# Kernel optimization log

Hardware: AMD Instinct MI355X
Metric: run time of the kernel (lower is better)

## Reference

```python
import jax, jax.numpy as jnp
import numpy as np


def setup_inputs() -> dict:
    key = jax.random.key(0)
    ks = jax.random.split(key, 6)
    B, HW, CIN, COUT, K = 256, 64, 3, 128, 32
    inputs = jax.random.normal(ks[0], (B, HW, HW, CIN), jnp.float32)
    conv_w = jax.random.normal(ks[1], (3, 3, CIN, COUT), jnp.float32) * 0.1
    conv_b = jnp.zeros((COUT,), jnp.float32)
    match_w = jax.random.normal(ks[2], (COUT,), jnp.float32) * 0.1
    match_b = jnp.zeros((1,), jnp.float32)
    pat_w = jax.random.normal(ks[3], (32 * 32 * K, 1), jnp.float32) * 0.01
    pat_b = jnp.zeros((1,), jnp.float32)
    base_w = jax.random.normal(ks[4], (32 * 32 * COUT, 3), jnp.float32) * 0.01
    base_b = jnp.zeros((3,), jnp.float32)
    pattern_set_index = jax.random.randint(ks[5], (K,), 0, COUT, jnp.int32)
    return {
        "inputs": inputs, "conv_w": conv_w, "conv_b": conv_b,
        "match_w": match_w, "match_b": match_b,
        "pat_w": pat_w, "pat_b": pat_b,
        "base_w": base_w, "base_b": base_b,
        "pattern_set_index": pattern_set_index,
    }


def reference(inputs, conv_w, conv_b, match_w, match_b,
              pat_w, pat_b, base_w, base_b, pattern_set_index):
    B = inputs.shape[0]
    # feat_extract: conv3x3 stride 2 + relu -> feats0 [B,32,32,128]; GAP -> feats1 [B,128]
    feats0 = jax.nn.relu(
        jax.lax.conv_general_dilated(
            inputs, conv_w, window_strides=(2, 2), padding='SAME',
            dimension_numbers=('NHWC', 'HWIO', 'NHWC')) + conv_b)
    feats1 = feats0.mean(axis=(1, 2))  # [B,128]
    # pat_matcher: boolean per-sample match mask
    matches = (feats1 @ match_w + match_b[0]) > 0.0  # [B] bool
    # pat_pred on channel-subset features (tf.gather axis=3)
    sel = jnp.take(feats0, pattern_set_index, axis=3)  # [B,32,32,32]
    p = jax.nn.sigmoid(sel.reshape(B, -1) @ pat_w + pat_b)[:, 0]  # [B]
    # BinaryToCategorical(pattern_class=0, num_classes=3): [p, (1-p)/2, (1-p)/2]
    o = (1.0 - p) * 0.5
    cat = jnp.stack([p, o, o], axis=-1)  # [B,3]
    # base_pred on full features (used for matched-low and non-matched samples)
    base = jax.nn.softmax(feats0.reshape(B, -1) @ base_w + base_b, axis=-1)  # [B,3]
    # route: matched AND pat score >= 0.5 -> categorized pat pred, else base pred
    use_pat = matches & (p >= 0.5)
    return jnp.where(use_pat[:, None], cat, base)
```

## Files before the change

### kernel.cpp

```cpp
#include <hip/hip_runtime.h>
#include <math.h>

#define TPB 1024

__global__ __launch_bounds__(256)
void prep_weights(const float* __restrict__ base_w,
                  const float* __restrict__ pat_w,
                  const int*   __restrict__ psi,
                  float4* __restrict__ wq)
{
    int idx = blockIdx.x * 256 + threadIdx.x;
    int hw = idx >> 7, c = idx & 127;
    const float* bp = base_w + (size_t)idx * 3;
    float b0 = bp[0], b1 = bp[1], b2 = bp[2];
    float pc = 0.f;
    const float* pr = pat_w + hw * 32;
    #pragma unroll
    for (int k = 0; k < 32; ++k)
        pc += (psi[k] == c) ? pr[k] : 0.f;
    wq[idx] = make_float4(b0, b1, b2, pc);
}

__global__ __launch_bounds__(TPB, 4)
void pattern_branch_kernel(const float* __restrict__ in,
                           const float* __restrict__ conv_w,
                           const float* __restrict__ conv_b,
                           const float* __restrict__ match_w,
                           const float* __restrict__ match_b,
                           const float* __restrict__ pat_b,
                           const float* __restrict__ base_b,
                           const float4* __restrict__ wq,
                           float* __restrict__ out)
{
    constexpr int ROWF4 = 50;
    __shared__ float4 xlds4[65 * ROWF4];
    __shared__ float  red[16][5];

    const int b   = blockIdx.x;
    const int tid = threadIdx.x;

    for (int s = tid; s < 65 * ROWF4; s += TPB) xlds4[s] = make_float4(0.f, 0.f, 0.f, 0.f);
    __syncthreads();
    const float4* inp4 = (const float4*)(in + (size_t)b * 12288);
    for (int s = tid; s < 64 * 48; s += TPB) {
        int r = s / 48;
        int q = s - r * 48;
        xlds4[r * ROWF4 + q] = inp4[s];
    }
    __syncthreads();

    const int lane31 = tid & 31;
    const int cg     = (tid >> 5) & 1;
    const int sg     = tid >> 6;
    const int c0     = lane31 + 32 * cg;
    float w[2][27], bias[2], mw[2];
    #pragma unroll
    for (int jj = 0; jj < 2; ++jj) {
        int c = c0 + 64 * jj;
        bias[jj] = conv_b[c];
        mw[jj]   = match_w[c];
        #pragma unroll
        for (int k = 0; k < 27; ++k) w[jj][k] = conv_w[k * 128 + c];
    }

    float s_match = 0.f, sb0 = 0.f, sb1 = 0.f, sb2 = 0.f, s_pat = 0.f;

    for (int it = 0; it < 16; ++it) {
        int slot = it * 16 + sg;
        int oh = slot >> 3;
        int q  = slot & 7;
        float acc[4][2];
        #pragma unroll
        for (int v = 0; v < 4; ++v) { acc[v][0] = bias[0]; acc[v][1] = bias[1]; }

        #pragma unroll
        for (int kh = 0; kh < 3; ++kh) {
            float xr[28];
            const float4* rp = &xlds4[(2 * oh + kh) * ROWF4 + 6 * q];
            #pragma unroll
            for (int u = 0; u < 7; ++u) {
                float4 v4 = rp[u];
                xr[4*u] = v4.x; xr[4*u+1] = v4.y; xr[4*u+2] = v4.z; xr[4*u+3] = v4.w;
            }
            #pragma unroll
            for (int v = 0; v < 4; ++v)
                #pragma unroll
                for (int t9 = 0; t9 < 9; ++t9) {
                    float xv = xr[6 * v + t9];
                    int k = kh * 9 + t9;
                    acc[v][0] = fmaf(xv, w[0][k], acc[v][0]);
                    acc[v][1] = fmaf(xv, w[1][k], acc[v][1]);
                }
        }
        #pragma unroll
        for (int v = 0; v < 4; ++v) {
            int hw = oh * 32 + 4 * q + v;
            const float4* wqp = wq + hw * 128 + c0;
            #pragma unroll
            for (int jj = 0; jj < 2; ++jj) {
                float fv = fmaxf(acc[v][jj], 0.f);
                float4 wv = wqp[64 * jj];
                s_match = fmaf(mw[jj], fv, s_match);
                sb0   = fmaf(fv, wv.x, sb0);
                sb1   = fmaf(fv, wv.y, sb1);
                sb2   = fmaf(fv, wv.z, sb2);
                s_pat = fmaf(fv, wv.w, s_pat);
            }
        }
    }

    float vals[5] = { s_match, sb0, sb1, sb2, s_pat };
    #pragma unroll
    for (int off = 32; off > 0; off >>= 1)
        #pragma unroll
        for (int v = 0; v < 5; ++v)
            vals[v] += __shfl_down(vals[v], off, 64);
    int wv = tid >> 6, lane = tid & 63;
    if (lane == 0) {
        #pragma unroll
        for (int v = 0; v < 5; ++v) red[wv][v] = vals[v];
    }
    __syncthreads();
    if (tid == 0) {
        float t[5] = {0.f, 0.f, 0.f, 0.f, 0.f};
        for (int wj = 0; wj < 16; ++wj)
            #pragma unroll
            for (int v = 0; v < 5; ++v) t[v] += red[wj][v];
        float score = t[0] * (1.f / 1024.f) + match_b[0];
        float p = 1.f / (1.f + expf(-(t[4] + pat_b[0])));
        float l0 = t[1] + base_b[0], l1 = t[2] + base_b[1], l2 = t[3] + base_b[2];
        float m = fmaxf(l0, fmaxf(l1, l2));
        float e0 = expf(l0 - m), e1 = expf(l1 - m), e2 = expf(l2 - m);
        float inv = 1.f / (e0 + e1 + e2);
        bool use_pat = (score > 0.f) && (p >= 0.5f);
        float o0, o1, o2;
        if (use_pat) { o0 = p; o1 = 0.5f * (1.f - p); o2 = o1; }
        else         { o0 = e0 * inv; o1 = e1 * inv; o2 = e2 * inv; }
        out[b * 3 + 0] = o0;
        out[b * 3 + 1] = o1;
        out[b * 3 + 2] = o2;
    }
}

extern "C" void kernel_launch(void* const* d_in, const int* in_sizes, int n_in,
                              void* d_out, int out_size, void* d_ws, size_t ws_size,
                              hipStream_t stream) {
    const float* in      = (const float*)d_in[0];
    const float* conv_w  = (const float*)d_in[1];
    const float* conv_b  = (const float*)d_in[2];
    const float* match_w = (const float*)d_in[3];
    const float* match_b = (const float*)d_in[4];
    const float* pat_w   = (const float*)d_in[5];
    const float* pat_b   = (const float*)d_in[6];
    const float* base_w  = (const float*)d_in[7];
    const float* base_b  = (const float*)d_in[8];
    const int*   psi     = (const int*)d_in[9];
    float* out = (float*)d_out;

    float4* wq = (float4*)d_ws;

    prep_weights<<<512, 256, 0, stream>>>(base_w, pat_w, psi, wq);

    int B = in_sizes[0] / (64 * 64 * 3);
    pattern_branch_kernel<<<B, TPB, 0, stream>>>(
        in, conv_w, conv_b, match_w, match_b, pat_b, base_b, wq, out);
}
```

Baseline: 116.2 us.

## Split each sample across four row-quarter blocks with separate finalize kernel

```diff
diff --git a/kernel.cpp b/kernel.cpp
--- a/kernel.cpp
+++ b/kernel.cpp
@@ -1,7 +1,7 @@
 #include <hip/hip_runtime.h>
 #include <math.h>
 
-#define TPB 1024
+#define TPB 512
 
 __global__ __launch_bounds__(256)
 void prep_weights(const float* __restrict__ base_w,
@@ -21,91 +21,86 @@
     wq[idx] = make_float4(b0, b1, b2, pc);
 }
 
-__global__ __launch_bounds__(TPB, 4)
+__global__ __launch_bounds__(TPB, 8)
 void pattern_branch_kernel(const float* __restrict__ in,
                            const float* __restrict__ conv_w,
                            const float* __restrict__ conv_b,
                            const float* __restrict__ match_w,
-                           const float* __restrict__ match_b,
-                           const float* __restrict__ pat_b,
-                           const float* __restrict__ base_b,
                            const float4* __restrict__ wq,
-                           float* __restrict__ out)
+                           float* __restrict__ part)
 {
     constexpr int ROWF4 = 50;
-    __shared__ float4 xlds4[65 * ROWF4];
-    __shared__ float  red[16][5];
+    __shared__ float4 xlds4[17 * ROWF4];
+    __shared__ float  red[8][5];
 
-    const int b   = blockIdx.x;
+    const int bx  = blockIdx.x;
+    const int qh  = bx >> 8;
+    const int b   = bx & 255;
     const int tid = threadIdx.x;
 
-    for (int s = tid; s < 65 * ROWF4; s += TPB) xlds4[s] = make_float4(0.f, 0.f, 0.f, 0.f);
+    for (int s = tid; s < 17 * ROWF4; s += TPB) xlds4[s] = make_float4(0.f, 0.f, 0.f, 0.f);
     __syncthreads();
     const float4* inp4 = (const float4*)(in + (size_t)b * 12288);
-    for (int s = tid; s < 64 * 48; s += TPB) {
-        int r = s / 48;
-        int q = s - r * 48;
-        xlds4[r * ROWF4 + q] = inp4[s];
+    for (int s = tid; s < 17 * 48; s += TPB) {
+        int r  = s / 48;
+        int qq = s - r * 48;
+        int ih = 16 * qh + r;
+        if (ih < 64) xlds4[r * ROWF4 + qq] = inp4[ih * 48 + qq];
     }
     __syncthreads();
 
-    const int lane31 = tid & 31;
-    const int cg     = (tid >> 5) & 1;
-    const int sg     = tid >> 6;
-    const int c0     = lane31 + 32 * cg;
-    float w[2][27], bias[2], mw[2];
+    const int c  = tid & 127;
+    const int sg = tid >> 7;
+    float w[27];
     #pragma unroll
-    for (int jj = 0; jj < 2; ++jj) {
-        int c = c0 + 64 * jj;
-        bias[jj] = conv_b[c];
-        mw[jj]   = match_w[c];
-        #pragma unroll
-        for (int k = 0; k < 27; ++k) w[jj][k] = conv_w[k * 128 + c];
-    }
+    for (int k = 0; k < 27; ++k) w[k] = conv_w[k * 128 + c];
+    const float bias = conv_b[c];
+    const float mw   = match_w[c];
 
     float s_match = 0.f, sb0 = 0.f, sb1 = 0.f, sb2 = 0.f, s_pat = 0.f;
 
     for (int it = 0; it < 16; ++it) {
-        int slot = it * 16 + sg;
-        int oh = slot >> 3;
-        int q  = slot & 7;
-        float acc[4][2];
-        #pragma unroll
-        for (int v = 0; v < 4; ++v) { acc[v][0] = bias[0]; acc[v][1] = bias[1]; }
+        int slot   = it * 4 + sg;
+        int oh_loc = slot >> 3;
+        int q      = slot & 7;
+        float acc[4] = { bias, bias, bias, bias };
 
         #pragma unroll
         for (int kh = 0; kh < 3; ++kh) {
-            float xr[28];
-            const float4* rp = &xlds4[(2 * oh + kh) * ROWF4 + 6 * q];
-            #pragma unroll
-            for (int u = 0; u < 7; ++u) {
-                float4 v4 = rp[u];
-                xr[4*u] = v4.x; xr[4*u+1] = v4.y; xr[4*u+2] = v4.z; xr[4*u+3] = v4.w;
-            }
-            #pragma unroll
-            for (int v = 0; v < 4; ++v)
+            const float4* rp = &xlds4[(2 * oh_loc + kh) * ROWF4 + 6 * q];
+            {
+                float4 t0 = rp[0], t1 = rp[1], t2 = rp[2], t3 = rp[3];
+                float x[16] = { t0.x,t0.y,t0.z,t0.w, t1.x,t1.y,t1.z,t1.w,
+                                t2.x,t2.y,t2.z,t2.w, t3.x,t3.y,t3.z,t3.w };
                 #pragma unroll
                 for (int t9 = 0; t9 < 9; ++t9) {
-                    float xv = xr[6 * v + t9];
-                    int k = kh * 9 + t9;
-                    acc[v][0] = fmaf(xv, w[0][k], acc[v][0]);
-                    acc[v][1] = fmaf(xv, w[1][k], acc[v][1]);
+                    float wk = w[kh * 9 + t9];
+                    acc[0] = fmaf(x[t9],     wk, acc[0]);
+                    acc[1] = fmaf(x[6 + t9], wk, acc[1]);
                 }
+            }
+            {
+                float4 t0 = rp[3], t1 = rp[4], t2 = rp[5], t3 = rp[6];
+                float x[16] = { t0.x,t0.y,t0.z,t0.w, t1.x,t1.y,t1.z,t1.w,
+                                t2.x,t2.y,t2.z,t2.w, t3.x,t3.y,t3.z,t3.w };
+                #pragma unroll
+                for (int t9 = 0; t9 < 9; ++t9) {
+                    float wk = w[kh * 9 + t9];
+                    acc[2] = fmaf(x[t9],     wk, acc[2]);
+                    acc[3] = fmaf(x[6 + t9], wk, acc[3]);
+                }
+            }
         }
+        int hwbase = (8 * qh + oh_loc) * 32 + 4 * q;
         #pragma unroll
         for (int v = 0; v < 4; ++v) {
-            int hw = oh * 32 + 4 * q + v;
-            const float4* wqp = wq + hw * 128 + c0;
-            #pragma unroll
-            for (int jj = 0; jj < 2; ++jj) {
-                float fv = fmaxf(acc[v][jj], 0.f);
-                float4 wv = wqp[64 * jj];
-                s_match = fmaf(mw[jj], fv, s_match);
-                sb0   = fmaf(fv, wv.x, sb0);
-                sb1   = fmaf(fv, wv.y, sb1);
-                sb2   = fmaf(fv, wv.z, sb2);
-                s_pat = fmaf(fv, wv.w, s_pat);
-            }
+            float fv = fmaxf(acc[v], 0.f);
+            float4 wv = wq[(size_t)(hwbase + v) * 128 + c];
+            s_match = fmaf(mw, fv, s_match);
+            sb0   = fmaf(fv, wv.x, sb0);
+            sb1   = fmaf(fv, wv.y, sb1);
+            sb2   = fmaf(fv, wv.z, sb2);
+            s_pat = fmaf(fv, wv.w, s_pat);
         }
     }
 
@@ -122,24 +117,42 @@
     }
     __syncthreads();
     if (tid == 0) {
-        float t[5] = {0.f, 0.f, 0.f, 0.f, 0.f};
-        for (int wj = 0; wj < 16; ++wj)
-            #pragma unroll
-            for (int v = 0; v < 5; ++v) t[v] += red[wj][v];
-        float score = t[0] * (1.f / 1024.f) + match_b[0];
-        float p = 1.f / (1.f + expf(-(t[4] + pat_b[0])));
-        float l0 = t[1] + base_b[0], l1 = t[2] + base_b[1], l2 = t[3] + base_b[2];
-        float m = fmaxf(l0, fmaxf(l1, l2));
-        float e0 = expf(l0 - m), e1 = expf(l1 - m), e2 = expf(l2 - m);
-        float inv = 1.f / (e0 + e1 + e2);
-        bool use_pat = (score > 0.f) && (p >= 0.5f);
-        float o0, o1, o2;
-        if (use_pat) { o0 = p; o1 = 0.5f * (1.f - p); o2 = o1; }
-        else         { o0 = e0 * inv; o1 = e1 * inv; o2 = e2 * inv; }
-        out[b * 3 + 0] = o0;
-        out[b * 3 + 1] = o1;
-        out[b * 3 + 2] = o2;
+        #pragma unroll
+        for (int v = 0; v < 5; ++v) {
+            float t = 0.f;
+            for (int wj = 0; wj < 8; ++wj) t += red[wj][v];
+            part[(qh * 5 + v) * 256 + b] = t;
+        }
     }
+}
+
+__global__ __launch_bounds__(256)
+void finalize_kernel(const float* __restrict__ part,
+                     const float* __restrict__ match_b,
+                     const float* __restrict__ pat_b,
+                     const float* __restrict__ base_b,
+                     float* __restrict__ out)
+{
+    int b = threadIdx.x;
+    float t[5] = { 0.f, 0.f, 0.f, 0.f, 0.f };
+    #pragma unroll
+    for (int j = 0; j < 4; ++j)
+        #pragma unroll
+        for (int v = 0; v < 5; ++v)
+            t[v] += part[(j * 5 + v) * 256 + b];
+    float score = t[0] * (1.f / 1024.f) + match_b[0];
+    float p = 1.f / (1.f + expf(-(t[4] + pat_b[0])));
+    float l0 = t[1] + base_b[0], l1 = t[2] + base_b[1], l2 = t[3] + base_b[2];
+    float m = fmaxf(l0, fmaxf(l1, l2));
+    float e0 = expf(l0 - m), e1 = expf(l1 - m), e2 = expf(l2 - m);
+    float inv = 1.f / (e0 + e1 + e2);
+    bool use_pat = (score > 0.f) && (p >= 0.5f);
+    float o0, o1, o2;
+    if (use_pat) { o0 = p; o1 = 0.5f * (1.f - p); o2 = o1; }
+    else         { o0 = e0 * inv; o1 = e1 * inv; o2 = e2 * inv; }
+    out[b * 3 + 0] = o0;
+    out[b * 3 + 1] = o1;
+    out[b * 3 + 2] = o2;
 }
 
 extern "C" void kernel_launch(void* const* d_in, const int* in_sizes, int n_in,
@@ -157,11 +170,14 @@
     const int*   psi     = (const int*)d_in[9];
     float* out = (float*)d_out;
 
-    float4* wq = (float4*)d_ws;
+    float4* wq   = (float4*)d_ws;
+    float*  part = (float*)((char*)d_ws + (size_t)131072 * 16);
 
     prep_weights<<<512, 256, 0, stream>>>(base_w, pat_w, psi, wq);
 
     int B = in_sizes[0] / (64 * 64 * 3);
-    pattern_branch_kernel<<<B, TPB, 0, stream>>>(
-        in, conv_w, conv_b, match_w, match_b, pat_b, base_b, wq, out);
+    pattern_branch_kernel<<<4 * B, TPB, 0, stream>>>(
+        in, conv_w, conv_b, match_w, wq, part);
+
+    finalize_kernel<<<1, 256, 0, stream>>>(part, match_b, pat_b, base_b, out);
 }
```

Result: no change. 118.4 us (+1.9%).
